# Kernel optimization log

Hardware: AMD Instinct MI355X
Metric: run time of the kernel (lower is better)

The kernel has to match this reference:

```python
import jax, jax.numpy as jnp
from jax import lax
import numpy as np

FL = 7      # filter_length (odd so each decomposition level preserves L)
LEVEL = 3
T = 5       # time_points
C = 64      # channels
HID = 64    # ODE hidden width (== C so ODE state shape is preserved)
TD = 16     # time embedding dim
REG = 0.01  # DyWAN reg_factor


def _gelu(x):
    return jax.nn.gelu(x, approximate=False)  # torch nn.GELU default = exact


def _conv1d(x, w, b, pad):
    # x [B,Cin,L], w [Cout,Cin,K] -> [B,Cout,L'] (cross-correlation, as torch)
    out = lax.conv_general_dilated(x, w, (1,), [(pad, pad)],
                                   dimension_numbers=('NCH', 'OIH', 'NCH'))
    return out + b[None, :, None]


def _dywan(x, w1, b1, wg1, bg1, wg2, bg2):
    # DyWAN_Pro: global stats -> dynamic lo/hi filters + regularizers
    stat = x.mean(-1)                                  # AdaptiveAvgPool1d(1)+Flatten
    h = _gelu(stat @ w1.T + b1)
    h = _gelu(h @ wg1.T + bg1)
    f = h @ wg2.T + bg2                                # [B, 2*FL]
    lo, hi = f[:, :FL], f[:, FL:]
    # smoothness: conv1d with kernel [-1,1], zero pad 1 -> xp[l+1]-xp[l]
    lp = jnp.pad(lo, ((0, 0), (1, 1)))
    lo_smooth = jnp.abs(lp[:, 1:] - lp[:, :-1]).mean()
    lo_n = lo / (jnp.linalg.norm(lo, axis=1, keepdims=True) + 1e-8)
    shift_loss = 0.0
    for s in (1, 2, 3):
        sh = jnp.roll(lo_n, s, axis=1)
        shift_loss = shift_loss + jnp.abs(lo_n[:, :, None] * sh[:, None, :]).mean()
    amp_loss = jnp.abs((lo_n ** 2).sum(1) - 1.0).mean()
    ortho = REG * (shift_loss + amp_loss)
    return lo, hi, ortho + lo_smooth * 0.1


def _batch_filter_conv(ap, filt):
    # per-sample depthwise conv: ap [B,C,L], filt [B,FL] -> [B,C,L]
    B, Ch, L = ap.shape
    pad = (FL - 1) // 2
    xp = jnp.pad(ap, ((0, 0), (0, 0), (pad, pad)), mode='edge')  # replicate pad
    xp = xp.reshape(1, B * Ch, L + 2 * pad)
    k = jnp.repeat(filt[:, None, :], Ch, axis=1).reshape(B * Ch, 1, FL)
    out = lax.conv_general_dilated(xp, k, (1,), 'VALID',
                                   dimension_numbers=('NCH', 'OIH', 'NCH'),
                                   feature_group_count=B * Ch)
    return out.reshape(B, Ch, -1)[..., :L]


def _adaptive_time_grid(sig):
    g = jnp.abs(jnp.diff(sig, axis=-1))                          # [B,C,L-1]
    gp = jnp.pad(g, ((0, 0), (0, 0), (2, 2)))                    # avg_pool1d k=5 pad=2
    cs = jnp.pad(jnp.cumsum(gp, axis=-1), ((0, 0), (0, 0), (1, 0)))
    inten = (cs[..., 5:] - cs[..., :-5]) / 5.0                   # [B,C,L-1]
    mn, mx = inten.min(), inten.max()
    td = jnp.where(mx - mn < 1e-8, 0.5,
                   (inten - mn) / (mx - mn + 1e-30) * 0.9 + 0.1)
    tg = jnp.concatenate([jnp.zeros_like(td[..., :1]),
                          jnp.cumsum(td[..., :-1], -1)], -1)     # time_grid
    tg = tg / jnp.maximum(tg.max(), 1e-12)
    idx = np.linspace(0, td.shape[-1] - 1, T).astype(np.int64)   # static indices
    return tg[..., idx].mean((0, 1))                             # [T], increasing


def reference(x, dy_w1, dy_b1, dy_wg1, dy_bg1, dy_wg2, dy_bg2,
              ode_c1w, ode_c1b, ode_c2w, ode_c2b, ode_wt, ode_bt,
              ode_wm, ode_bm, ode_emb,
              gate_w, gate_b, attn1_w, attn1_b, attn2_w, attn2_b):
    # ---- multi-level dynamic wavelet decomposition ----
    coeffs = [x]
    approx = x
    ortho = jnp.float32(0.0)
    for _ in range(LEVEL):
        lo, hi, ortho = _dywan(approx, dy_w1, dy_b1, dy_wg1, dy_bg1, dy_wg2, dy_bg2)
        new_approx = _batch_filter_conv(approx, lo)
        detail = _batch_filter_conv(approx, hi)
        coeffs.append(detail)
        approx = new_approx
    coeffs[0] = approx

    # ---- per-scale ODE evolution: RK4 over the adaptive time grid ----
    def ode_f(t, y, lvl):
        h = _conv1d(y, ode_c1w[lvl], ode_c1b[lvl], 1)
        h = _gelu(h)
        h = _conv1d(h, ode_c2w[lvl], ode_c2b[lvl], 1)
        temb = jax.nn.silu(ode_wt[lvl][:, 0] * t + ode_bt[lvl])   # [TD]
        gb = ode_wm[lvl] @ temb + ode_bm[lvl]                     # [2*HID]
        gamma, beta = gb[:HID], gb[HID:]
        se = ode_emb[lvl, lvl]                                    # scale embedding
        mod = h * (1.0 + gamma + se)[None, :, None] + beta[None, :, None]
        return jax.nn.silu(mod) - 0.1 * y                         # PhysicsActivation

    evolved = []
    for lvl in range(LEVEL + 1):
        c = coeffs[lvl]
        ts = _adaptive_time_grid(c)
        y = c
        for j in range(T - 1):
            t0, t1 = ts[j], ts[j + 1]
            dt = t1 - t0
            k1 = ode_f(t0, y, lvl)
            k2 = ode_f(t0 + dt / 2, y + dt / 2 * k1, lvl)
            k3 = ode_f(t0 + dt / 2, y + dt / 2 * k2, lvl)
            k4 = ode_f(t1, y + dt * k3, lvl)
            y = y + dt / 6 * (k1 + 2 * k2 + 2 * k3 + k4)
        e_in = jnp.mean(c ** 2, axis=(1, 2), keepdims=True)
        e_out = jnp.mean(y ** 2, axis=(1, 2), keepdims=True)
        evolved.append(y * jnp.sqrt(e_in / (e_out + 1e-8)))       # energy constraint

    # ---- gated cross-scale fusion ----
    current = evolved[0]
    yh = evolved[1:]
    enhanced = []
    for i in range(LEVEL - 1, -1, -1):
        detail = yh[i]
        if i < LEVEL - 1:
            a = _gelu(_conv1d(current, attn1_w[i], attn1_b[i], 0))
            a = jax.nn.sigmoid(_conv1d(a, attn2_w[i], attn2_b[i], 0))
            detail = detail * a + detail
        gate = jax.nn.sigmoid(_conv1d(current, gate_w[i], gate_b[i], 1))
        current = current + gate * detail
        enhanced.append(detail)
    enhanced.reverse()
    out = jnp.stack([current] + enhanced, axis=0)   # [LEVEL+1, B, C, L] = (yl, yh...)
    return out, ortho


def setup_inputs() -> dict:
    key = jax.random.key(0)
    ks = jax.random.split(key, 16)
    B, L = 8, 2048

    def rn(k, shape, sc=0.1):
        return jax.random.normal(k, shape, dtype=jnp.float32) * sc

    return {
        'x': jax.random.normal(ks[0], (B, C, L), dtype=jnp.float32),
        'dy_w1': rn(ks[1], (HID, C)),
        'dy_b1': jnp.zeros((HID,), jnp.float32),
        'dy_wg1': rn(ks[2], (2 * HID, HID)),
        'dy_bg1': jnp.zeros((2 * HID,), jnp.float32),
        'dy_wg2': rn(ks[3], (2 * FL, 2 * HID)),
        'dy_bg2': rn(ks[4], (2 * FL,), 0.1),
        'ode_c1w': rn(ks[5], (LEVEL + 1, HID, C, 3)),
        'ode_c1b': jnp.zeros((LEVEL + 1, HID), jnp.float32),
        'ode_c2w': rn(ks[6], (LEVEL + 1, HID, HID, 3)),
        'ode_c2b': jnp.zeros((LEVEL + 1, HID), jnp.float32),
        'ode_wt': rn(ks[7], (LEVEL + 1, TD, 1)),
        'ode_bt': jnp.zeros((LEVEL + 1, TD), jnp.float32),
        'ode_wm': rn(ks[8], (LEVEL + 1, 2 * HID, TD)),
        'ode_bm': jnp.zeros((LEVEL + 1, 2 * HID), jnp.float32),
        'ode_emb': rn(ks[9], (LEVEL + 1, 8, HID)),
        'gate_w': rn(ks[10], (LEVEL, C, C, 3)),
        'gate_b': jnp.zeros((LEVEL, C), jnp.float32),
        'attn1_w': rn(ks[11], (LEVEL - 1, C // 4, C, 1)),
        'attn1_b': jnp.zeros((LEVEL - 1, C // 4), jnp.float32),
        'attn2_w': rn(ks[12], (LEVEL - 1, C, C // 4, 1)),
        'attn2_b': jnp.zeros((LEVEL - 1, C), jnp.float32),
    }
```

## Files before the change

kernel.cpp:

```cpp
#include <hip/hip_runtime.h>
#include <math.h>

#define LSEQ 2048
#define NB 8
#define NCH 64
#define NTOT (NB*NCH*LSEQ)
#define NROWS (NB*NCH)

typedef __attribute__((ext_vector_type(8))) short short8;
typedef __attribute__((ext_vector_type(4))) float float4v;

__device__ __forceinline__ float geluf(float x){
    return 0.5f*x*(1.0f+erff(x*0.70710678118654752f));
}
__device__ __forceinline__ float siluf(float x){
    return x/(1.0f+expf(-x));
}
__device__ __forceinline__ float sigf(float x){
    return 1.0f/(1.0f+expf(-x));
}
__device__ __forceinline__ unsigned short f2bf(float f){
    unsigned u=__float_as_uint(f);
    u += 0x7fffu + ((u>>16)&1u);
    return (unsigned short)(u>>16);
}
__device__ __forceinline__ float bf2f(unsigned h){
    return __uint_as_float((h&0xffffu)<<16);
}

__global__ __launch_bounds__(256) void wtrans_kernel(const float* __restrict__ w,
                                                     float* __restrict__ wt){
    int idx = blockIdx.x*256 + threadIdx.x;
    int j = idx >> 6, co = idx & 63;
    wt[idx] = w[co*192 + j];
}

__global__ __launch_bounds__(256) void wprep_kernel(const float* __restrict__ c1w,
                                                    const float* __restrict__ c2w,
                                                    short* __restrict__ WB){
    int idx = blockIdx.x*256 + threadIdx.x;
    if (idx >= 196608) return;
    int ci  = idx & 63;
    int co  = (idx>>6) & 63;
    int tap = (idx>>12) % 3;
    int st  = (idx/(3<<12)) & 1;
    int lvl = idx/(6<<12);
    const float* src = (st==0? c1w : c2w);
    float w = src[(size_t)lvl*12288 + co*192 + ci*3 + tap];
    unsigned short hi = f2bf(w);
    float lo = w - bf2f(hi);
    size_t base = ((((size_t)(lvl*2+st)*2+0)*3+tap)*64+co)*64+ci;
    size_t basl = ((((size_t)(lvl*2+st)*2+1)*3+tap)*64+co)*64+ci;
    WB[base] = (short)hi;
    WB[basl] = (short)f2bf(lo);
}

__global__ __launch_bounds__(256) void stat_kernel(const float* __restrict__ in,
                                                   float* __restrict__ stat){
    int r = blockIdx.x, tid = threadIdx.x;
    const float* p = in + (size_t)r*LSEQ;
    float acc = 0.f;
    for (int i=tid;i<LSEQ;i+=256) acc += p[i];
    for (int o=32;o>0;o>>=1) acc += __shfl_down(acc,o,64);
    __shared__ float red[4];
    if ((tid&63)==0) red[tid>>6]=acc;
    __syncthreads();
    if (tid==0) stat[r] = red[0]+red[1]+red[2]+red[3];
}

__global__ __launch_bounds__(256) void dywan_kernel(
    float* __restrict__ stat,
    const float* __restrict__ w1, const float* __restrict__ b1,
    const float* __restrict__ wg1, const float* __restrict__ bg1,
    const float* __restrict__ wg2, const float* __restrict__ bg2,
    float* __restrict__ lo_out, float* __restrict__ hi_out,
    float* __restrict__ ortho_out)
{
    __shared__ float st[512];
    __shared__ float h1s[512];
    __shared__ float h2s[1024];
    __shared__ float fs[112];
    int tid = threadIdx.x;
    for (int i=tid;i<512;i+=256) st[i]=stat[i]*(1.0f/LSEQ);
    __syncthreads();
    for (int i=tid;i<512;i+=256) stat[i]=0.f;
    for (int idx=tid; idx<512; idx+=256){
        int b=idx>>6, j=idx&63;
        float acc=b1[j];
        const float* W=w1+j*64;
        for (int i=0;i<64;i++) acc += st[b*64+i]*W[i];
        h1s[idx]=geluf(acc);
    }
    __syncthreads();
    for (int idx=tid; idx<1024; idx+=256){
        int b=idx>>7, j=idx&127;
        float acc=bg1[j];
        const float* W=wg1+j*64;
        for (int i=0;i<64;i++) acc += h1s[b*64+i]*W[i];
        h2s[idx]=geluf(acc);
    }
    __syncthreads();
    if (tid<112){
        int b=tid/14, j=tid-b*14;
        float acc=bg2[j];
        const float* W=wg2+j*128;
        for (int i=0;i<128;i++) acc += h2s[b*128+i]*W[i];
        fs[tid]=acc;
    }
    __syncthreads();
    if (tid<56){
        int b=tid/7, k=tid-b*7;
        lo_out[tid]=fs[b*14+k];
        hi_out[tid]=fs[b*14+7+k];
    }
    if (tid==0){
        float smooth=0.f, shiftsum=0.f, ampsum=0.f;
        for (int b=0;b<8;b++){
            const float* l = fs + b*14;
            float prev=0.f, nrm=0.f;
            for (int k=0;k<7;k++){ smooth += fabsf(l[k]-prev); prev=l[k]; nrm += l[k]*l[k]; }
            smooth += fabsf(prev);
            float denom = sqrtf(nrm) + 1e-8f;
            float sabs=0.f, s2=0.f;
            for (int k=0;k<7;k++){ float v=l[k]/denom; sabs+=fabsf(v); s2+=v*v; }
            shiftsum += sabs*sabs;
            ampsum += fabsf(s2-1.0f);
        }
        smooth *= (1.0f/64.0f);
        float shift = 3.0f*shiftsum/(8.0f*49.0f);
        float amp = ampsum*(1.0f/8.0f);
        *ortho_out = 0.01f*(shift+amp) + 0.1f*smooth;
    }
}

__global__ __launch_bounds__(256) void filt_kernel(
    const float* __restrict__ ap, const float* __restrict__ lo,
    const float* __restrict__ hi, float* __restrict__ na,
    float* __restrict__ det, float* __restrict__ stat_out)
{
    int r = blockIdx.y, l0 = blockIdx.x*256, tid = threadIdx.x;
    int b = r>>6;
    __shared__ float s[262];
    __shared__ float fl[7], fh[7];
    __shared__ float sred[4];
    for (int idx=tid; idx<262; idx+=256){
        int l = l0+idx-3;
        l = min(max(l,0),LSEQ-1);
        s[idx]=ap[(size_t)r*LSEQ+l];
    }
    if (tid<7) fl[tid]=lo[b*7+tid];
    else if (tid<14) fh[tid-7]=hi[b*7+tid-7];
    __syncthreads();
    float a=0.f, d=0.f;
    #pragma unroll
    for (int k=0;k<7;k++){ float v=s[tid+k]; a+=v*fl[k]; d+=v*fh[k]; }
    na[(size_t)r*LSEQ+l0+tid]=a;
    det[(size_t)r*LSEQ+l0+tid]=d;
    if (stat_out){
        float sm=a;
        for (int o=32;o>0;o>>=1) sm += __shfl_down(sm,o,64);
        if ((tid&63)==0) sred[tid>>6]=sm;
        __syncthreads();
        if (tid==0) atomicAdd(&stat_out[r], sred[0]+sred[1]+sred[2]+sred[3]);
    }
}

__global__ __launch_bounds__(256) void tg_pass1(const float* __restrict__ CB,
                                                float* __restrict__ rowstats){
    __shared__ float sh[2048];
    __shared__ float red[28];
    int r = blockIdx.x, lvl = blockIdx.y, tid = threadIdx.x;
    const float* s = CB + (size_t)lvl*NTOT + (size_t)r*LSEQ;
    float* rso = rowstats + (size_t)(lvl*NROWS+r)*8;
    for (int i=tid;i<2048;i+=256) sh[i]=s[i];
    __syncthreads();
    float ssq=0.f;
    for (int i=tid;i<2048;i+=256){ float v=sh[i]; ssq+=v*v; }
    float mn=1e30f, mx=-1e30f, s0=0.f,s1=0.f,s2=0.f,s3=0.f;
    for (int j=tid;j<2047;j+=256){
        int k0 = (j-2>0)? j-2:0;
        int k1 = (j+2<2046)? j+2:2046;
        float acc=0.f;
        for (int k=k0;k<=k1;k++) acc += fabsf(sh[k+1]-sh[k]);
        float inten = acc*0.2f;
        mn=fminf(mn,inten); mx=fmaxf(mx,inten);
        if (j<511)  s0+=inten;
        if (j<1023) s1+=inten;
        if (j<1534) s2+=inten;
        if (j<2046) s3+=inten;
    }
    float vals[7]={mn,mx,s0,s1,s2,s3,ssq};
    for (int o=32;o>0;o>>=1){
        vals[0]=fminf(vals[0],__shfl_down(vals[0],o,64));
        vals[1]=fmaxf(vals[1],__shfl_down(vals[1],o,64));
        vals[2]+=__shfl_down(vals[2],o,64);
        vals[3]+=__shfl_down(vals[3],o,64);
        vals[4]+=__shfl_down(vals[4],o,64);
        vals[5]+=__shfl_down(vals[5],o,64);
        vals[6]+=__shfl_down(vals[6],o,64);
    }
    int lane=tid&63, w=tid>>6;
    if (lane==0) for (int q=0;q<7;q++) red[w*7+q]=vals[q];
    __syncthreads();
    if (tid==0){
        rso[0]=fminf(fminf(red[0],red[7]),fminf(red[14],red[21]));
        rso[1]=fmaxf(fmaxf(red[1],red[8]),fmaxf(red[15],red[22]));
        rso[2]=red[2]+red[9]+red[16]+red[23];
        rso[3]=red[3]+red[10]+red[17]+red[24];
        rso[4]=red[4]+red[11]+red[18]+red[25];
        rso[5]=red[5]+red[12]+red[19]+red[26];
        rso[6]=red[6]+red[13]+red[20]+red[27];
    }
}

__global__ __launch_bounds__(256) void tg_finalize(
    const float* __restrict__ rowstats,
    const float* __restrict__ wt, const float* __restrict__ bt,
    const float* __restrict__ wm, const float* __restrict__ bm,
    const float* __restrict__ emb,
    float* __restrict__ ts_out, float* __restrict__ modsc,
    float* __restrict__ modbi, float* __restrict__ ein,
    float* __restrict__ eout)
{
    int tid=threadIdx.x;
    const int lvl=blockIdx.x;
    const float* rs = rowstats + (size_t)lvl*NROWS*8;
    __shared__ float red[28];
    __shared__ float stv[9];
    __shared__ float temb[144];
    float mn=1e30f,mx=-1e30f,a0=0.f,a1=0.f,a2=0.f,a3=0.f,m3=-1e30f;
    for (int r=tid;r<512;r+=256){
        mn=fminf(mn,rs[r*8+0]); mx=fmaxf(mx,rs[r*8+1]);
        a0+=rs[r*8+2]; a1+=rs[r*8+3]; a2+=rs[r*8+4]; a3+=rs[r*8+5];
        m3=fmaxf(m3,rs[r*8+5]);
    }
    float vals[7]={mn,mx,a0,a1,a2,a3,m3};
    for (int o=32;o>0;o>>=1){
        vals[0]=fminf(vals[0],__shfl_down(vals[0],o,64));
        vals[1]=fmaxf(vals[1],__shfl_down(vals[1],o,64));
        vals[2]+=__shfl_down(vals[2],o,64);
        vals[3]+=__shfl_down(vals[3],o,64);
        vals[4]+=__shfl_down(vals[4],o,64);
        vals[5]+=__shfl_down(vals[5],o,64);
        vals[6]=fmaxf(vals[6],__shfl_down(vals[6],o,64));
    }
    int lane=tid&63, w=tid>>6;
    if (lane==0) for (int q=0;q<7;q++) red[w*7+q]=vals[q];
    if (tid<8){
        float e=0.f;
        for (int c=0;c<64;c++) e += rs[(tid*64+c)*8+6];
        ein[lvl*8+tid]=e*(1.0f/131072.0f);
        eout[lvl*8+tid]=0.f;
    }
    __syncthreads();
    if (tid==0){
        float mnv=fminf(fminf(red[0],red[7]),fminf(red[14],red[21]));
        float mxv=fmaxf(fmaxf(red[1],red[8]),fmaxf(red[15],red[22]));
        float s0=red[2]+red[9]+red[16]+red[23];
        float s1=red[3]+red[10]+red[17]+red[24];
        float s2=red[4]+red[11]+red[18]+red[25];
        float s3=red[5]+red[12]+red[19]+red[26];
        float m3v=fmaxf(fmaxf(red[6],red[13]),fmaxf(red[20],red[27]));
        const float idxs[5]={0.f,511.f,1023.f,1534.f,2046.f};
        float tsv[5];
        if (mxv-mnv < 1e-8f){
            for (int k=0;k<5;k++) tsv[k]=idxs[k]/2046.0f;
        } else {
            float a = 0.9f/(mxv-mnv+1e-30f);
            float bb = 0.1f - a*mnv;
            float gmax = a*m3v + bb*2046.0f;
            float sums[5]={0.f,s0,s1,s2,s3};
            tsv[0]=0.f;
            for (int k=1;k<5;k++)
                tsv[k]=(a*(sums[k]*(1.0f/512.0f)) + bb*idxs[k])/gmax;
        }
        for (int k=0;k<5;k++){ ts_out[lvl*8+k]=tsv[k]; stv[2*k]=tsv[k]; }
        for (int k=0;k<4;k++) stv[2*k+1]=tsv[k] + 0.5f*(tsv[k+1]-tsv[k]);
    }
    __syncthreads();
    if (tid<144){
        int m=tid>>4, i=tid&15;
        float z = wt[lvl*16+i]*stv[m] + bt[lvl*16+i];
        temb[tid]=siluf(z);
    }
    __syncthreads();
    for (int idx=tid; idx<1152; idx+=256){
        int m=idx>>7, c=idx&127;
        float g=bm[lvl*128+c];
        const float* W=wm+(size_t)(lvl*128+c)*16;
        const float* te=temb+m*16;
        for (int i=0;i<16;i++) g += W[i]*te[i];
        if (c<64) modsc[lvl*576+m*64+c]=1.0f+g+emb[(lvl*8+lvl)*64+c];
        else      modbi[lvl*576+m*64+(c-64)]=g;
    }
}

__global__ __launch_bounds__(256) void ode_eval_all(
    const float* __restrict__ yinB, const unsigned* __restrict__ kprevB,
    unsigned* __restrict__ koutB, const unsigned* __restrict__ accrdB,
    unsigned* __restrict__ accB,
    float* __restrict__ youtB,
    const short* __restrict__ WB, const float* __restrict__ c1bB,
    const float* __restrict__ c2bB,
    const float* __restrict__ modscB, const float* __restrict__ modbiB,
    const float* __restrict__ tsB, float* __restrict__ eoutB,
    int step, int eval, int do_energy)
{
    __shared__ unsigned yTh[68][36];
    __shared__ unsigned yTl[68][36];
    __shared__ unsigned hTh[66][36];
    __shared__ float red[4];
    const int tid=threadIdx.x;
    const int lvl=blockIdx.z;
    const int b=blockIdx.y;
    const int l0=blockIdx.x*64;
    const size_t loff=(size_t)lvl*NTOT;
    const size_t loffP=(size_t)lvl*(NTOT/2);
    const float* yin = yinB + loff;
    const unsigned* kprev = kprevB + loffP;
    unsigned* kout = koutB + loffP;
    const unsigned* accrd = accrdB + loffP;
    unsigned* acc = accB + loffP;
    float* yout = youtB + loff;
    const float dt = tsB[lvl*8+step+1]-tsB[lvl*8+step];
    const float alpha=(eval==0)?0.f:((eval==3)?dt:0.5f*dt);
    const int tslot=2*step+((eval==0)?0:((eval==3)?2:1));
    const int wv=tid>>6, lane=tid&63;
    const int n=lane&15, quad=lane>>4;
    const int m0=wv*16;

    #pragma unroll
    for (int pass=0; pass<2; pass++){
        int r = pass*64 + lane;
        if (r < 68){
            int l = l0 - 2 + r;
            bool ok = (l>=0 && l<LSEQ);
            #pragma unroll
            for (int qq=0; qq<8; qq++){
                int q = wv*8 + qq;
                float v0=0.f, v1=0.f;
                if (ok){
                    size_t g0=(size_t)(b*64+2*q)*LSEQ+l;
                    v0=yin[g0]; v1=yin[g0+LSEQ];
                    if (eval!=0){
                        unsigned ku = kprev[((size_t)(b*32+q))*LSEQ + l];
                        v0 += alpha*bf2f(ku);
                        v1 += alpha*bf2f(ku>>16);
                    }
                }
                unsigned short h0=f2bf(v0), h1=f2bf(v1);
                yTh[r][q] = (unsigned)h0 | ((unsigned)h1<<16);
                yTl[r][q] = (unsigned)f2bf(v0-bf2f(h0)) | ((unsigned)f2bf(v1-bf2f(h1))<<16);
            }
        }
    }
    __syncthreads();

    {
        const short* W1 = WB + (size_t)(lvl*2+0)*2*3*4096;
        short8 A[3][2][2];
        #pragma unroll
        for (int tap=0;tap<3;tap++)
            #pragma unroll
            for (int ks=0;ks<2;ks++)
                #pragma unroll
                for (int hl=0;hl<2;hl++)
                    A[tap][ks][hl] = *(const short8*)(W1 + (((size_t)hl*3+tap)*64 + (m0+n))*64 + ks*32 + quad*8);
        float bia[4];
        #pragma unroll
        for (int reg=0;reg<4;reg++) bia[reg]=c1bB[lvl*64 + m0 + quad*4 + reg];
        const int q0=(m0>>1)+quad*2;
        #pragma unroll
        for (int nt=0; nt<5; nt++){
            float4v d = {bia[0],bia[1],bia[2],bia[3]};
            #pragma unroll
            for (int tap=0;tap<3;tap++){
                int rr = 16*nt + n + tap;
                rr = (rr>67)? 67 : rr;
                const unsigned* ph=&yTh[rr][0];
                const unsigned* pl=&yTl[rr][0];
                #pragma unroll
                for (int ks=0;ks<2;ks++){
                    short8 bh = *(const short8*)(ph + ks*16 + quad*4);
                    short8 bl = *(const short8*)(pl + ks*16 + quad*4);
                    d = __builtin_amdgcn_mfma_f32_16x16x32_bf16(A[tap][ks][0], bh, d, 0,0,0);
                    d = __builtin_amdgcn_mfma_f32_16x16x32_bf16(A[tap][ks][0], bl, d, 0,0,0);
                    d = __builtin_amdgcn_mfma_f32_16x16x32_bf16(A[tap][ks][1], bh, d, 0,0,0);
                }
            }
            if (nt<4 || n<2){
                int rh = 16*nt + n;
                int hpos = l0 - 1 + rh;
                bool okh = (hpos>=0 && hpos<LSEQ);
                float h0 = okh? geluf(d[0]) : 0.f;
                float h1 = okh? geluf(d[1]) : 0.f;
                float h2 = okh? geluf(d[2]) : 0.f;
                float h3 = okh? geluf(d[3]) : 0.f;
                hTh[rh][q0]   = (unsigned)f2bf(h0) | ((unsigned)f2bf(h1)<<16);
                hTh[rh][q0+1] = (unsigned)f2bf(h2) | ((unsigned)f2bf(h3)<<16);
            }
        }
    }
    __syncthreads();

    float esum=0.f;
    {
        const short* W2 = WB + (size_t)(lvl*2+1)*2*3*4096;
        short8 A[3][2][2];
        #pragma unroll
        for (int tap=0;tap<3;tap++)
            #pragma unroll
            for (int ks=0;ks<2;ks++)
                #pragma unroll
                for (int hl=0;hl<2;hl++)
                    A[tap][ks][hl] = *(const short8*)(W2 + (((size_t)hl*3+tap)*64 + (m0+n))*64 + ks*32 + quad*8);
        float bib[4], sc[4], bi2[4];
        #pragma unroll
        for (int reg=0;reg<4;reg++){
            int co = m0 + quad*4 + reg;
            bib[reg]=c2bB[lvl*64+co];
            sc[reg]=modscB[lvl*576+tslot*64+co];
            bi2[reg]=modbiB[lvl*576+tslot*64+co];
        }
        const float dt6 = dt/6.0f;
        const int qy0=(m0+quad*4)>>1;
        #pragma unroll
        for (int nt=0; nt<4; nt++){
            float4v d = {bib[0],bib[1],bib[2],bib[3]};
            #pragma unroll
            for (int tap=0;tap<3;tap++){
                const int rr = 16*nt + n + tap;
                const unsigned* ph=&hTh[rr][0];
                #pragma unroll
                for (int ks=0;ks<2;ks++){
                    short8 bh = *(const short8*)(ph + ks*16 + quad*4);
                    d = __builtin_amdgcn_mfma_f32_16x16x32_bf16(A[tap][ks][0], bh, d, 0,0,0);
                    d = __builtin_amdgcn_mfma_f32_16x16x32_bf16(A[tap][ks][1], bh, d, 0,0,0);
                }
            }
            int p = l0 + 16*nt + n;
            int ry = 16*nt + n + 2;
            unsigned uh0=yTh[ry][qy0],   ul0=yTl[ry][qy0];
            unsigned uh1=yTh[ry][qy0+1], ul1=yTl[ry][qy0+1];
            float yev[4];
            yev[0]=bf2f(uh0)+bf2f(ul0);
            yev[1]=bf2f(uh0>>16)+bf2f(ul0>>16);
            yev[2]=bf2f(uh1)+bf2f(ul1);
            yev[3]=bf2f(uh1>>16)+bf2f(ul1>>16);
            float kv[4];
            #pragma unroll
            for (int reg=0;reg<4;reg++){
                float m = d[reg]*sc[reg] + bi2[reg];
                kv[reg] = siluf(m) - 0.1f*yev[reg];
            }
            size_t ia = ((size_t)(b*32+qy0))*LSEQ + p;
            size_t ib = ia + LSEQ;
            if (eval==0){
                kout[ia]=(unsigned)f2bf(kv[0])|((unsigned)f2bf(kv[1])<<16);
                kout[ib]=(unsigned)f2bf(kv[2])|((unsigned)f2bf(kv[3])<<16);
            } else if (eval<3){
                unsigned ka=(unsigned)f2bf(kv[0])|((unsigned)f2bf(kv[1])<<16);
                unsigned kb=(unsigned)f2bf(kv[2])|((unsigned)f2bf(kv[3])<<16);
                kout[ia]=ka; kout[ib]=kb;
                unsigned ua=accrd[ia], ub=accrd[ib];
                float a0=bf2f(ua)+2.f*kv[0],     a1=bf2f(ua>>16)+2.f*kv[1];
                float a2=bf2f(ub)+2.f*kv[2],     a3=bf2f(ub>>16)+2.f*kv[3];
                acc[ia]=(unsigned)f2bf(a0)|((unsigned)f2bf(a1)<<16);
                acc[ib]=(unsigned)f2bf(a2)|((unsigned)f2bf(a3)<<16);
            } else {
                unsigned ua=accrd[ia], ub=accrd[ib];
                float av[4]={bf2f(ua),bf2f(ua>>16),bf2f(ub),bf2f(ub>>16)};
                size_t gbase=(size_t)(b*64 + m0 + quad*4)*LSEQ + p;
                #pragma unroll
                for (int reg=0;reg<4;reg++){
                    size_t gi = gbase + (size_t)reg*LSEQ;
                    float yn = yin[gi] + dt6*(av[reg]+kv[reg]);
                    yout[gi]=yn;
                    esum += yn*yn;
                }
            }
        }
    }
    if (do_energy){
        for (int o=32;o>0;o>>=1) esum+=__shfl_down(esum,o,64);
        if ((tid&63)==0) red[tid>>6]=esum;
        __syncthreads();
        if (tid==0) atomicAdd(&eoutB[lvl*8+b], red[0]+red[1]+red[2]+red[3]);
    }
}

__global__ __launch_bounds__(256) void recon_kernel(
    const float* __restrict__ cur, const float* __restrict__ det_in,
    float* __restrict__ det_out,
    const float* __restrict__ a1w, const float* __restrict__ a1b,
    const float* __restrict__ a2w, const float* __restrict__ a2b,
    const float* __restrict__ gwt, const float* __restrict__ gb,
    float* __restrict__ curout,
    const float* __restrict__ ein, const float* __restrict__ eout,
    int lvl_cur, int lvl_det, int has_attn)
{
    __shared__ float yc[64][66];
    __shared__ float dtile[64][65];
    __shared__ float hid[16][64];
    const int tid=threadIdx.x, b=blockIdx.y, l0=blockIdx.x*64;
    float scur=1.f, sdet;
    if (lvl_cur>=0){
        float eo=eout[lvl_cur*8+b]*(1.0f/131072.0f);
        scur=sqrtf(ein[lvl_cur*8+b]/(eo+1e-8f));
    }
    {
        float eo=eout[lvl_det*8+b]*(1.0f/131072.0f);
        sdet=sqrtf(ein[lvl_det*8+b]/(eo+1e-8f));
    }
    for (int idx=tid; idx<64*66; idx+=256){
        int ci=idx/66, u=idx-ci*66;
        int l=l0+u-1;
        yc[ci][u]=(l>=0 && l<LSEQ)? scur*cur[(size_t)(b*64+ci)*LSEQ+l] : 0.f;
    }
    for (int idx=tid; idx<4096; idx+=256){
        int ci=idx>>6, p=idx&63;
        dtile[ci][p]=sdet*det_in[(size_t)(b*64+ci)*LSEQ+l0+p];
    }
    __syncthreads();
    if (has_attn){
        for (int idx=tid; idx<1024; idx+=256){
            int h=idx>>6, p=idx&63;
            float acc=a1b[h];
            const float* W=a1w+h*64;
            for (int ci=0;ci<64;ci++) acc += W[ci]*yc[ci][p+1];
            hid[h][p]=geluf(acc);
        }
        __syncthreads();
        for (int idx=tid; idx<4096; idx+=256){
            int co=idx>>6, p=idx&63;
            float acc=a2b[co];
            const float* W=a2w+co*16;
            #pragma unroll
            for (int h=0;h<16;h++) acc += W[h]*hid[h][p];
            float a=sigf(acc);
            float dnew = dtile[co][p]*(1.0f+a);
            dtile[co][p]=dnew;
            det_out[(size_t)(b*64+co)*LSEQ+l0+p]=dnew;
        }
        __syncthreads();
    } else {
        for (int idx=tid; idx<4096; idx+=256){
            int ci=idx>>6, p=idx&63;
            det_out[(size_t)(b*64+ci)*LSEQ+l0+p]=dtile[ci][p];
        }
    }
    const int co=tid&63, g=tid>>6;
    const int p0=g*16;
    float a[16];
    float bb=gb[co];
    #pragma unroll
    for (int i=0;i<16;i++) a[i]=bb;
    for (int ci=0;ci<64;ci++){
        float w0=gwt[(ci*3+0)*64+co];
        float w1_=gwt[(ci*3+1)*64+co];
        float w2_=gwt[(ci*3+2)*64+co];
        float x[18];
        #pragma unroll
        for (int j=0;j<18;j++) x[j]=yc[ci][p0+j];
        #pragma unroll
        for (int i=0;i<16;i++) a[i] += w0*x[i]+w1_*x[i+1]+w2_*x[i+2];
    }
    float r[16];
    #pragma unroll
    for (int i=0;i<16;i++){
        float gt=sigf(a[i]);
        r[i]=yc[co][p0+i+1]+gt*dtile[co][p0+i];
    }
    __syncthreads();
    #pragma unroll
    for (int i=0;i<16;i++) dtile[co][p0+i]=r[i];
    __syncthreads();
    for (int idx=tid; idx<4096; idx+=256){
        int ci=idx>>6, p=idx&63;
        curout[(size_t)(b*64+ci)*LSEQ+l0+p]=dtile[ci][p];
    }
}

extern "C" void kernel_launch(void* const* d_in, const int* in_sizes, int n_in,
                              void* d_out, int out_size, void* d_ws, size_t ws_size,
                              hipStream_t stream)
{
    (void)in_sizes; (void)n_in; (void)out_size; (void)ws_size;
    const float* x       =(const float*)d_in[0];
    const float* dy_w1   =(const float*)d_in[1];
    const float* dy_b1   =(const float*)d_in[2];
    const float* dy_wg1  =(const float*)d_in[3];
    const float* dy_bg1  =(const float*)d_in[4];
    const float* dy_wg2  =(const float*)d_in[5];
    const float* dy_bg2  =(const float*)d_in[6];
    const float* ode_c1w =(const float*)d_in[7];
    const float* ode_c1b =(const float*)d_in[8];
    const float* ode_c2w =(const float*)d_in[9];
    const float* ode_c2b =(const float*)d_in[10];
    const float* ode_wt  =(const float*)d_in[11];
    const float* ode_bt  =(const float*)d_in[12];
    const float* ode_wm  =(const float*)d_in[13];
    const float* ode_bm  =(const float*)d_in[14];
    const float* ode_emb =(const float*)d_in[15];
    const float* gate_w  =(const float*)d_in[16];
    const float* gate_b  =(const float*)d_in[17];
    const float* attn1_w =(const float*)d_in[18];
    const float* attn1_b =(const float*)d_in[19];
    const float* attn2_w =(const float*)d_in[20];
    const float* attn2_b =(const float*)d_in[21];
    float* out=(float*)d_out;
    float* ws=(float*)d_ws;
    const size_t N=NTOT;
    float* CB = ws;
    float* PB = ws+4*N;
    float* QB = ws+8*N;
    unsigned* K0P=(unsigned*)(ws+12*N);
    unsigned* K1P=(unsigned*)(ws+14*N);
    unsigned* ACP=(unsigned*)(ws+16*N);
    float* SM = ws+20*N;
    float* stat_ws =SM;
    float* lo_ws   =SM+512;
    float* hi_ws   =SM+576;
    float* rowstats=SM+1024;
    float* ts_ws   =SM+17408;
    float* modsc   =SM+17536;
    float* modbi   =SM+19840;
    float* ein     =SM+22144;
    float* eoutb   =SM+22176;
    short* WB      =(short*)(SM+24576);
    float* WTG     =SM+24576+196608;

    dim3 blk(256);

    wprep_kernel<<<768,blk,0,stream>>>(ode_c1w, ode_c2w, WB);
    for (int i=0;i<3;i++)
        wtrans_kernel<<<48,blk,0,stream>>>(gate_w+(size_t)i*12288, WTG+(size_t)i*12288);

    stat_kernel<<<NROWS,blk,0,stream>>>(x, stat_ws);
    const float* cura=x;
    float* outsA[3]={PB, PB+N, CB};
    float* outsD[3]={CB+N, CB+2*N, CB+3*N};
    for (int lv=0; lv<3; lv++){
        dywan_kernel<<<1,blk,0,stream>>>(stat_ws, dy_w1,dy_b1,dy_wg1,dy_bg1,dy_wg2,dy_bg2,
                                         lo_ws, hi_ws, out+4*N);
        float* statn = (lv<2)? stat_ws : nullptr;
        filt_kernel<<<dim3(8,NROWS),blk,0,stream>>>(cura, lo_ws, hi_ws,
                                                    outsA[lv], outsD[lv], statn);
        cura=outsA[lv];
    }

    tg_pass1<<<dim3(NROWS,4),blk,0,stream>>>(CB, rowstats);
    tg_finalize<<<4,blk,0,stream>>>(rowstats, ode_wt, ode_bt, ode_wm, ode_bm,
                                    ode_emb, ts_ws, modsc, modbi, ein, eoutb);

    const float* yins[4]={CB, PB, QB, PB};
    float*       youts[4]={PB, QB, PB, QB};
    for (int step=0;step<4;step++){
        for (int ev=0;ev<4;ev++){
            const unsigned* kp=(ev==2)? K1P : K0P;
            unsigned* ko=(ev==1)? K1P : K0P;
            const unsigned* ar=(ev==1)? K0P : ACP;
            int doe=(step==3 && ev==3)?1:0;
            ode_eval_all<<<dim3(32,NB,4),blk,0,stream>>>(
                yins[step],kp,ko,ar,ACP,youts[step],
                WB,ode_c1b,ode_c2b,modsc,modbi,ts_ws,eoutb,step,ev,doe);
        }
    }

    recon_kernel<<<dim3(32,NB),blk,0,stream>>>(QB+0*N, QB+3*N, out+3*N,
        attn1_w, attn1_b, attn2_w, attn2_b,
        WTG+2*12288, gate_b+128, PB, ein, eoutb, 0, 3, 0);
    recon_kernel<<<dim3(32,NB),blk,0,stream>>>(PB, QB+2*N, out+2*N,
        attn1_w+1024, attn1_b+16, attn2_w+1024, attn2_b+64,
        WTG+1*12288, gate_b+64, QB, ein, eoutb, -1, 2, 1);
    recon_kernel<<<dim3(32,NB),blk,0,stream>>>(QB, QB+1*N, out+1*N,
        attn1_w, attn1_b, attn2_w, attn2_b,
        WTG, gate_b, out+0*N, ein, eoutb, -1, 1, 1);
}
```

Before: 744.6 us.

## Fuse four RK4 stage evaluations into one kernel with halo recompute

```diff
diff --git a/kernel.cpp b/kernel.cpp
--- a/kernel.cpp
+++ b/kernel.cpp
@@ -295,45 +295,36 @@
     }
 }
 
-__global__ __launch_bounds__(256) void ode_eval_all(
-    const float* __restrict__ yinB, const unsigned* __restrict__ kprevB,
-    unsigned* __restrict__ koutB, const unsigned* __restrict__ accrdB,
-    unsigned* __restrict__ accB,
-    float* __restrict__ youtB,
+__global__ __launch_bounds__(256) void ode_rk4_step(
+    const float* __restrict__ yinB, float* __restrict__ youtB,
     const short* __restrict__ WB, const float* __restrict__ c1bB,
     const float* __restrict__ c2bB,
     const float* __restrict__ modscB, const float* __restrict__ modbiB,
     const float* __restrict__ tsB, float* __restrict__ eoutB,
-    int step, int eval, int do_energy)
+    int step, int do_energy)
 {
-    __shared__ unsigned yTh[68][36];
-    __shared__ unsigned yTl[68][36];
-    __shared__ unsigned hTh[66][36];
+    __shared__ unsigned Yh[80][36], Yl[80][36];
+    __shared__ unsigned Eh[80][36], El[80][36];
+    __shared__ unsigned Hh[80][36];
     __shared__ float red[4];
     const int tid=threadIdx.x;
-    const int lvl=blockIdx.z;
-    const int b=blockIdx.y;
+    const int lvl=blockIdx.z, b=blockIdx.y;
     const int l0=blockIdx.x*64;
     const size_t loff=(size_t)lvl*NTOT;
-    const size_t loffP=(size_t)lvl*(NTOT/2);
     const float* yin = yinB + loff;
-    const unsigned* kprev = kprevB + loffP;
-    unsigned* kout = koutB + loffP;
-    const unsigned* accrd = accrdB + loffP;
-    unsigned* acc = accB + loffP;
     float* yout = youtB + loff;
     const float dt = tsB[lvl*8+step+1]-tsB[lvl*8+step];
-    const float alpha=(eval==0)?0.f:((eval==3)?dt:0.5f*dt);
-    const int tslot=2*step+((eval==0)?0:((eval==3)?2:1));
+    const float dt6 = dt*(1.0f/6.0f);
     const int wv=tid>>6, lane=tid&63;
     const int n=lane&15, quad=lane>>4;
     const int m0=wv*16;
+    const int qy0=(m0+quad*4)>>1;
 
     #pragma unroll
     for (int pass=0; pass<2; pass++){
         int r = pass*64 + lane;
-        if (r < 68){
-            int l = l0 - 2 + r;
+        if (r < 80){
+            int l = l0 - 8 + r;
             bool ok = (l>=0 && l<LSEQ);
             #pragma unroll
             for (int qq=0; qq<8; qq++){
@@ -342,106 +333,110 @@
                 if (ok){
                     size_t g0=(size_t)(b*64+2*q)*LSEQ+l;
                     v0=yin[g0]; v1=yin[g0+LSEQ];
-                    if (eval!=0){
-                        unsigned ku = kprev[((size_t)(b*32+q))*LSEQ + l];
-                        v0 += alpha*bf2f(ku);
-                        v1 += alpha*bf2f(ku>>16);
-                    }
                 }
                 unsigned short h0=f2bf(v0), h1=f2bf(v1);
-                yTh[r][q] = (unsigned)h0 | ((unsigned)h1<<16);
-                yTl[r][q] = (unsigned)f2bf(v0-bf2f(h0)) | ((unsigned)f2bf(v1-bf2f(h1))<<16);
+                Yh[r][q] = (unsigned)h0 | ((unsigned)h1<<16);
+                Yl[r][q] = (unsigned)f2bf(v0-bf2f(h0)) | ((unsigned)f2bf(v1-bf2f(h1))<<16);
             }
         }
     }
-    __syncthreads();
-
-    {
-        const short* W1 = WB + (size_t)(lvl*2+0)*2*3*4096;
-        short8 A[3][2][2];
+
+    const short* W1 = WB + (size_t)(lvl*2+0)*2*3*4096;
+    const short* W2 = WB + (size_t)(lvl*2+1)*2*3*4096;
+    short8 A1[3][2][2], A2[3][2][2];
+    #pragma unroll
+    for (int tap=0;tap<3;tap++)
         #pragma unroll
-        for (int tap=0;tap<3;tap++)
+        for (int ks=0;ks<2;ks++)
             #pragma unroll
-            for (int ks=0;ks<2;ks++)
-                #pragma unroll
-                for (int hl=0;hl<2;hl++)
-                    A[tap][ks][hl] = *(const short8*)(W1 + (((size_t)hl*3+tap)*64 + (m0+n))*64 + ks*32 + quad*8);
-        float bia[4];
+            for (int hl=0;hl<2;hl++){
+                size_t off = (((size_t)hl*3+tap)*64 + (m0+n))*64 + ks*32 + quad*8;
+                A1[tap][ks][hl] = *(const short8*)(W1 + off);
+                A2[tap][ks][hl] = *(const short8*)(W2 + off);
+            }
+    float bia[4], bib[4];
+    #pragma unroll
+    for (int reg=0;reg<4;reg++){
+        bia[reg]=c1bB[lvl*64 + m0 + quad*4 + reg];
+        bib[reg]=c2bB[lvl*64 + m0 + quad*4 + reg];
+    }
+    float acc[5][4];
+    #pragma unroll
+    for (int nt=0;nt<5;nt++)
         #pragma unroll
-        for (int reg=0;reg<4;reg++) bia[reg]=c1bB[lvl*64 + m0 + quad*4 + reg];
-        const int q0=(m0>>1)+quad*2;
+        for (int reg=0;reg<4;reg++) acc[nt][reg]=0.f;
+
+    __syncthreads();
+
+    float esum=0.f;
+    #pragma unroll 1
+    for (int e=0;e<4;e++){
+        const unsigned (*Sh)[36] = (e==0)? Yh : Eh;
+        const unsigned (*Sl)[36] = (e==0)? Yl : El;
+        const int hLo=2*e+1, hHi=79-2*e;
+        const int kLo=2*e+2, kHi=78-2*e;
+
         #pragma unroll
         for (int nt=0; nt<5; nt++){
             float4v d = {bia[0],bia[1],bia[2],bia[3]};
             #pragma unroll
             for (int tap=0;tap<3;tap++){
-                int rr = 16*nt + n + tap;
-                rr = (rr>67)? 67 : rr;
-                const unsigned* ph=&yTh[rr][0];
-                const unsigned* pl=&yTl[rr][0];
+                int rr = 16*nt + n + tap - 1;
+                rr = (rr<0)?0:((rr>79)?79:rr);
+                const unsigned* ph=&Sh[rr][0];
+                const unsigned* pl=&Sl[rr][0];
                 #pragma unroll
                 for (int ks=0;ks<2;ks++){
                     short8 bh = *(const short8*)(ph + ks*16 + quad*4);
                     short8 bl = *(const short8*)(pl + ks*16 + quad*4);
-                    d = __builtin_amdgcn_mfma_f32_16x16x32_bf16(A[tap][ks][0], bh, d, 0,0,0);
-                    d = __builtin_amdgcn_mfma_f32_16x16x32_bf16(A[tap][ks][0], bl, d, 0,0,0);
-                    d = __builtin_amdgcn_mfma_f32_16x16x32_bf16(A[tap][ks][1], bh, d, 0,0,0);
+                    d = __builtin_amdgcn_mfma_f32_16x16x32_bf16(A1[tap][ks][0], bh, d, 0,0,0);
+                    d = __builtin_amdgcn_mfma_f32_16x16x32_bf16(A1[tap][ks][0], bl, d, 0,0,0);
+                    d = __builtin_amdgcn_mfma_f32_16x16x32_bf16(A1[tap][ks][1], bh, d, 0,0,0);
                 }
             }
-            if (nt<4 || n<2){
-                int rh = 16*nt + n;
-                int hpos = l0 - 1 + rh;
-                bool okh = (hpos>=0 && hpos<LSEQ);
-                float h0 = okh? geluf(d[0]) : 0.f;
-                float h1 = okh? geluf(d[1]) : 0.f;
-                float h2 = okh? geluf(d[2]) : 0.f;
-                float h3 = okh? geluf(d[3]) : 0.f;
-                hTh[rh][q0]   = (unsigned)f2bf(h0) | ((unsigned)f2bf(h1)<<16);
-                hTh[rh][q0+1] = (unsigned)f2bf(h2) | ((unsigned)f2bf(h3)<<16);
-            }
-        }
-    }
-    __syncthreads();
-
-    float esum=0.f;
-    {
-        const short* W2 = WB + (size_t)(lvl*2+1)*2*3*4096;
-        short8 A[3][2][2];
-        #pragma unroll
-        for (int tap=0;tap<3;tap++)
-            #pragma unroll
-            for (int ks=0;ks<2;ks++)
-                #pragma unroll
-                for (int hl=0;hl<2;hl++)
-                    A[tap][ks][hl] = *(const short8*)(W2 + (((size_t)hl*3+tap)*64 + (m0+n))*64 + ks*32 + quad*8);
-        float bib[4], sc[4], bi2[4];
+            int R = 16*nt + n;
+            int hp = l0 - 8 + R;
+            bool okh = (R>=hLo && R<hHi && hp>=0 && hp<LSEQ);
+            float h0 = okh? geluf(d[0]) : 0.f;
+            float h1 = okh? geluf(d[1]) : 0.f;
+            float h2 = okh? geluf(d[2]) : 0.f;
+            float h3 = okh? geluf(d[3]) : 0.f;
+            Hh[R][qy0]   = (unsigned)f2bf(h0) | ((unsigned)f2bf(h1)<<16);
+            Hh[R][qy0+1] = (unsigned)f2bf(h2) | ((unsigned)f2bf(h3)<<16);
+        }
+        __syncthreads();
+
+        const int tslot = 2*step + ((e==0)?0:((e==3)?2:1));
+        float sc[4], bi2[4];
         #pragma unroll
         for (int reg=0;reg<4;reg++){
             int co = m0 + quad*4 + reg;
-            bib[reg]=c2bB[lvl*64+co];
-            sc[reg]=modscB[lvl*576+tslot*64+co];
+            sc[reg] =modscB[lvl*576+tslot*64+co];
             bi2[reg]=modbiB[lvl*576+tslot*64+co];
         }
-        const float dt6 = dt/6.0f;
-        const int qy0=(m0+quad*4)>>1;
+        const float alf = (e==2)? dt : 0.5f*dt;
+        const float wk  = (e==0)? 1.f : 2.f;
         #pragma unroll
-        for (int nt=0; nt<4; nt++){
+        for (int nt=0; nt<5; nt++){
             float4v d = {bib[0],bib[1],bib[2],bib[3]};
             #pragma unroll
             for (int tap=0;tap<3;tap++){
-                const int rr = 16*nt + n + tap;
-                const unsigned* ph=&hTh[rr][0];
+                int rr = 16*nt + n + tap - 1;
+                rr = (rr<0)?0:((rr>79)?79:rr);
+                const unsigned* ph=&Hh[rr][0];
                 #pragma unroll
                 for (int ks=0;ks<2;ks++){
                     short8 bh = *(const short8*)(ph + ks*16 + quad*4);
-                    d = __builtin_amdgcn_mfma_f32_16x16x32_bf16(A[tap][ks][0], bh, d, 0,0,0);
-                    d = __builtin_amdgcn_mfma_f32_16x16x32_bf16(A[tap][ks][1], bh, d, 0,0,0);
+                    d = __builtin_amdgcn_mfma_f32_16x16x32_bf16(A2[tap][ks][0], bh, d, 0,0,0);
+                    d = __builtin_amdgcn_mfma_f32_16x16x32_bf16(A2[tap][ks][1], bh, d, 0,0,0);
                 }
             }
-            int p = l0 + 16*nt + n;
-            int ry = 16*nt + n + 2;
-            unsigned uh0=yTh[ry][qy0],   ul0=yTl[ry][qy0];
-            unsigned uh1=yTh[ry][qy0+1], ul1=yTl[ry][qy0+1];
+            int R = 16*nt + n;
+            int p = l0 - 8 + R;
+            bool okp = (p>=0 && p<LSEQ);
+            bool okk = okp && R>=kLo && R<kHi;
+            unsigned uh0=Sh[R][qy0],   ul0=Sl[R][qy0];
+            unsigned uh1=Sh[R][qy0+1], ul1=Sl[R][qy0+1];
             float yev[4];
             yev[0]=bf2f(uh0)+bf2f(ul0);
             yev[1]=bf2f(uh0>>16)+bf2f(ul0>>16);
@@ -453,33 +448,35 @@
                 float m = d[reg]*sc[reg] + bi2[reg];
                 kv[reg] = siluf(m) - 0.1f*yev[reg];
             }
-            size_t ia = ((size_t)(b*32+qy0))*LSEQ + p;
-            size_t ib = ia + LSEQ;
-            if (eval==0){
-                kout[ia]=(unsigned)f2bf(kv[0])|((unsigned)f2bf(kv[1])<<16);
-                kout[ib]=(unsigned)f2bf(kv[2])|((unsigned)f2bf(kv[3])<<16);
-            } else if (eval<3){
-                unsigned ka=(unsigned)f2bf(kv[0])|((unsigned)f2bf(kv[1])<<16);
-                unsigned kb=(unsigned)f2bf(kv[2])|((unsigned)f2bf(kv[3])<<16);
-                kout[ia]=ka; kout[ib]=kb;
-                unsigned ua=accrd[ia], ub=accrd[ib];
-                float a0=bf2f(ua)+2.f*kv[0],     a1=bf2f(ua>>16)+2.f*kv[1];
-                float a2=bf2f(ub)+2.f*kv[2],     a3=bf2f(ub>>16)+2.f*kv[3];
-                acc[ia]=(unsigned)f2bf(a0)|((unsigned)f2bf(a1)<<16);
-                acc[ib]=(unsigned)f2bf(a2)|((unsigned)f2bf(a3)<<16);
-            } else {
-                unsigned ua=accrd[ia], ub=accrd[ib];
-                float av[4]={bf2f(ua),bf2f(ua>>16),bf2f(ub),bf2f(ub>>16)};
+            bool central = (R>=8 && R<72);
+            if (e<3){
+                unsigned vh0=Yh[R][qy0],   vl0=Yl[R][qy0];
+                unsigned vh1=Yh[R][qy0+1], vl1=Yl[R][qy0+1];
+                float z0 = okk? (bf2f(vh0)+bf2f(vl0)         + alf*kv[0]) : 0.f;
+                float z1 = okk? (bf2f(vh0>>16)+bf2f(vl0>>16) + alf*kv[1]) : 0.f;
+                float z2 = okk? (bf2f(vh1)+bf2f(vl1)         + alf*kv[2]) : 0.f;
+                float z3 = okk? (bf2f(vh1>>16)+bf2f(vl1>>16) + alf*kv[3]) : 0.f;
+                unsigned short e0=f2bf(z0), e1=f2bf(z1), e2=f2bf(z2), e3=f2bf(z3);
+                Eh[R][qy0]   = (unsigned)e0 | ((unsigned)e1<<16);
+                El[R][qy0]   = (unsigned)f2bf(z0-bf2f(e0)) | ((unsigned)f2bf(z1-bf2f(e1))<<16);
+                Eh[R][qy0+1] = (unsigned)e2 | ((unsigned)e3<<16);
+                El[R][qy0+1] = (unsigned)f2bf(z2-bf2f(e2)) | ((unsigned)f2bf(z3-bf2f(e3))<<16);
+                if (central){
+                    #pragma unroll
+                    for (int reg=0;reg<4;reg++) acc[nt][reg] += wk*kv[reg];
+                }
+            } else if (central){
                 size_t gbase=(size_t)(b*64 + m0 + quad*4)*LSEQ + p;
                 #pragma unroll
                 for (int reg=0;reg<4;reg++){
                     size_t gi = gbase + (size_t)reg*LSEQ;
-                    float yn = yin[gi] + dt6*(av[reg]+kv[reg]);
+                    float yn = yin[gi] + dt6*(acc[nt][reg] + kv[reg]);
                     yout[gi]=yn;
                     esum += yn*yn;
                 }
             }
         }
+        __syncthreads();
     }
     if (do_energy){
         for (int o=32;o>0;o>>=1) esum+=__shfl_down(esum,o,64);
@@ -614,9 +611,6 @@
     float* CB = ws;
     float* PB = ws+4*N;
     float* QB = ws+8*N;
-    unsigned* K0P=(unsigned*)(ws+12*N);
-    unsigned* K1P=(unsigned*)(ws+14*N);
-    unsigned* ACP=(unsigned*)(ws+16*N);
     float* SM = ws+20*N;
     float* stat_ws =SM;
     float* lo_ws   =SM+512;
@@ -655,16 +649,10 @@
 
     const float* yins[4]={CB, PB, QB, PB};
     float*       youts[4]={PB, QB, PB, QB};
-    for (int step=0;step<4;step++){
-        for (int ev=0;ev<4;ev++){
-            const unsigned* kp=(ev==2)? K1P : K0P;
-            unsigned* ko=(ev==1)? K1P : K0P;
-            const unsigned* ar=(ev==1)? K0P : ACP;
-            int doe=(step==3 && ev==3)?1:0;
-            ode_eval_all<<<dim3(32,NB,4),blk,0,stream>>>(
-                yins[step],kp,ko,ar,ACP,youts[step],
-                WB,ode_c1b,ode_c2b,modsc,modbi,ts_ws,eoutb,step,ev,doe);
-        }
+    for (int s=0;s<4;s++){
+        ode_rk4_step<<<dim3(32,NB,4),blk,0,stream>>>(
+            yins[s], youts[s], WB, ode_c1b, ode_c2b,
+            modsc, modbi, ts_ws, eoutb, s, (s==3)?1:0);
     }
 
     recon_kernel<<<dim3(32,NB),blk,0,stream>>>(QB+0*N, QB+3*N, out+3*N,
```

After: 823.3 us. +10.6%, slower.
